# Kernel tuning notes

Hardware: AMD Instinct MI355X
Metric: run time of the kernel (lower is better)

The kernel has to match this reference:

```python
import jax, jax.numpy as jnp
import numpy as np

N, E, F_IN, D, B = 20000, 50000, 16, 64, 128


def setup_inputs() -> dict:
    key = jax.random.key(0)
    ks = jax.random.split(key, 24)
    s = 0.05
    inp = {
        "x": jax.random.normal(ks[0], (N, F_IN), jnp.float32),
        "edge_index": jax.random.randint(ks[1], (2, E), 0, N, jnp.int32),
        "edge_attr": jax.random.uniform(ks[2], (E, 5), jnp.float32),
        "batch": jnp.sort(jax.random.randint(ks[3], (N,), 0, B, jnp.int32)),
        # lin0
        "lin0_w": jax.random.normal(ks[4], (D, F_IN)) * s,
        "lin0_b": jnp.zeros((D,), jnp.float32),
        # edge MLP: Linear(5,128) -> ReLU -> Linear(128, D*D)
        "mlp_w1": jax.random.normal(ks[5], (128, 5)) * s,
        "mlp_b1": jnp.zeros((128,), jnp.float32),
        "mlp_w2": jax.random.normal(ks[6], (D * D, 128)) * s,
        "mlp_b2": jnp.zeros((D * D,), jnp.float32),
        # NNConv bias (root_weight=False, bias=True)
        "conv_b": jnp.zeros((D,), jnp.float32),
        # GRU(dim, dim), single layer
        "gru_w_ih": jax.random.normal(ks[7], (3 * D, D)) * s,
        "gru_w_hh": jax.random.normal(ks[8], (3 * D, D)) * s,
        "gru_b_ih": jnp.zeros((3 * D,), jnp.float32),
        "gru_b_hh": jnp.zeros((3 * D,), jnp.float32),
        # Set2Set LSTM(2*dim, dim)
        "lstm_w_ih": jax.random.normal(ks[9], (4 * D, 2 * D)) * s,
        "lstm_w_hh": jax.random.normal(ks[10], (4 * D, D)) * s,
        "lstm_b_ih": jnp.zeros((4 * D,), jnp.float32),
        "lstm_b_hh": jnp.zeros((4 * D,), jnp.float32),
    }
    return inp


def _gru_cell(x, h, w_ih, w_hh, b_ih, b_hh):
    gi = x @ w_ih.T + b_ih
    gh = h @ w_hh.T + b_hh
    i_r, i_z, i_n = jnp.split(gi, 3, axis=-1)
    h_r, h_z, h_n = jnp.split(gh, 3, axis=-1)
    r = jax.nn.sigmoid(i_r + h_r)
    z = jax.nn.sigmoid(i_z + h_z)
    n = jnp.tanh(i_n + r * h_n)
    return (1.0 - z) * n + z * h


def _lstm_cell(x, h, c, w_ih, w_hh, b_ih, b_hh):
    g = x @ w_ih.T + b_ih + h @ w_hh.T + b_hh
    i, f, gg, o = jnp.split(g, 4, axis=-1)
    c_new = jax.nn.sigmoid(f) * c + jax.nn.sigmoid(i) * jnp.tanh(gg)
    h_new = jax.nn.sigmoid(o) * jnp.tanh(c_new)
    return h_new, c_new


def reference(x, edge_index, edge_attr, batch,
              lin0_w, lin0_b, mlp_w1, mlp_b1, mlp_w2, mlp_b2, conv_b,
              gru_w_ih, gru_w_hh, gru_b_ih, gru_b_hh,
              lstm_w_ih, lstm_w_hh, lstm_b_ih, lstm_b_hh):
    src, dst = edge_index[0], edge_index[1]

    out = jax.nn.relu(x @ lin0_w.T + lin0_b)  # [N, D]
    h = out  # GRU hidden (seq_len=1 -> out == h after each step)

    # Edge-conditioned weights: MLP(edge_attr) -> [E, D, D]
    hidden = jax.nn.relu(edge_attr @ mlp_w1.T + mlp_b1)
    W_e = (hidden @ mlp_w2.T + mlp_b2).reshape(E, D, D)

    # in-degree counts for mean aggregation
    deg = jax.ops.segment_sum(jnp.ones((E,), x.dtype), dst, num_segments=N)
    deg = jnp.maximum(deg, 1.0)[:, None]

    for _ in range(3):
        # NNConv: gather src feats, per-edge matmul, scatter-mean to dst
        msg = jnp.einsum('ed,edo->eo', out[src], W_e)  # [E, D]
        agg = jax.ops.segment_sum(msg, dst, num_segments=N) / deg
        m = jax.nn.relu(agg + conv_b)
        h = _gru_cell(m, h, gru_w_ih, gru_w_hh, gru_b_ih, gru_b_hh)
        out = h

    # Set2Set pooling, 3 processing steps
    q_star = jnp.zeros((B, 2 * D), x.dtype)
    hh = jnp.zeros((B, D), x.dtype)
    cc = jnp.zeros((B, D), x.dtype)
    for _ in range(3):
        hh, cc = _lstm_cell(q_star, hh, cc, lstm_w_ih, lstm_w_hh, lstm_b_ih, lstm_b_hh)
        q = hh  # [B, D]
        e = jnp.sum(out * q[batch], axis=-1)  # [N]
        e_max = jax.ops.segment_max(e, batch, num_segments=B)
        a = jnp.exp(e - e_max[batch])
        a = a / jax.ops.segment_sum(a, batch, num_segments=B)[batch]
        r = jax.ops.segment_sum(a[:, None] * out, batch, num_segments=B)  # [B, D]
        q_star = jnp.concatenate([q, r], axis=-1)

    return q_star  # [B, 2*D]
```

## Files before the change

### kernel.cpp

```cpp
#include <hip/hip_runtime.h>
#include <hip/hip_bf16.h>

typedef float BF;
__device__ __forceinline__ float ldf(const BF* p, int i) { return p[i]; }

typedef _Float16 h8 __attribute__((ext_vector_type(8)));
typedef float f4 __attribute__((ext_vector_type(4)));

static constexpr int N_NODES = 20000;
static constexpr int N_EDGES = 50000;
static constexpr int E_PAD   = 50176;
static constexpr int N_MSGB  = 392;
static constexpr int N_PAD   = 20032;
static constexpr int BROW    = 136;
static constexpr int SROW    = 72;
static constexpr int N_B     = 79;
static constexpr int MAXSEG  = 2048;

__device__ __forceinline__ float sigf(float x) { return 1.f / (1.f + __expf(-x)); }
__device__ __forceinline__ float tanh_f(float x) {
  float e = __expf(2.f * x);
  return 1.f - 2.f / (e + 1.f);
}

static constexpr int S1_LIN0 = 5000;
static constexpr int S1_QS   = 2048;
static constexpr int S1_WCAT = 128;
static constexpr int S1_B2S  = 16;
static constexpr int S1_DEG  = 196;
static constexpr int PREP1_BLOCKS = S1_LIN0 + S1_QS + S1_WCAT + S1_B2S + 1 + 1 + S1_DEG;

__global__ void k_prep1(const BF* __restrict__ x, const int* __restrict__ batch,
                        const int* __restrict__ dst,
                        const BF* __restrict__ w0, const BF* __restrict__ b0,
                        const BF* __restrict__ w2, const BF* __restrict__ b2,
                        const BF* __restrict__ gwih, const BF* __restrict__ gwhh,
                        const BF* __restrict__ gbih, const BF* __restrict__ gbhh,
                        float* __restrict__ h, _Float16* __restrict__ h16,
                        _Float16* __restrict__ Qs, _Float16* __restrict__ Wcat,
                        float* __restrict__ bcat, _Float16* __restrict__ b2s,
                        int* __restrict__ seg, int* __restrict__ degi,
                        int* __restrict__ bsum) {
  int bid = blockIdx.x, t = threadIdx.x;
  if (bid < S1_LIN0) {
    __shared__ float xs[64];
    if (t < 64) xs[t] = ldf(x, bid * 64 + t);
    __syncthreads();
    int nl = t >> 6, o = t & 63;
    float acc = ldf(b0, o);
#pragma unroll
    for (int f = 0; f < 16; ++f) acc += xs[nl * 16 + f] * ldf(w0, o * 16 + f);
    float v = fmaxf(acc, 0.f);
    int idx = bid * 256 + t;
    h[idx] = v;
    h16[idx] = (_Float16)v;
    return;
  }
  bid -= S1_LIN0;
  if (bid < S1_QS) {
    int idx = bid * 256 + t;
#pragma unroll
    for (int rep = 0; rep < 1; ++rep) {
      int i = idx;
      int dl = i >> 13, rem = i & 8191;
      int f = rem >> 9, ln = (rem >> 3) & 63, j = i & 7;
      int o = (f & 3) * 16 + (ln & 15);
      int k = (f >> 2) * 32 + (ln >> 4) * 8 + j;
      Qs[i] = (_Float16)ldf(w2, (dl * 64 + o) * 128 + k);
    }
    return;
  }
  bid -= S1_QS;
  if (bid < S1_WCAT) {
    int idx = bid * 256 + t, row = idx >> 7, k = idx & 127;
    int g = row >> 6, rr = row & 63;
    float v = 0.f;
    if (g == 0) v = (k < 64) ? ldf(gwih, rr * 64 + k) : ldf(gwhh, rr * 64 + (k - 64));
    else if (g == 1) v = (k < 64) ? ldf(gwih, (64 + rr) * 64 + k) : ldf(gwhh, (64 + rr) * 64 + (k - 64));
    else if (g == 2) v = (k < 64) ? ldf(gwih, (128 + rr) * 64 + k) : 0.f;
    else v = (k < 64) ? 0.f : ldf(gwhh, (128 + rr) * 64 + (k - 64));
    Wcat[idx] = (_Float16)v;
    return;
  }
  bid -= S1_WCAT;
  if (bid < S1_B2S) {
    int idx = bid * 256 + t;
    int f = idx >> 9, ln = (idx >> 3) & 63, j = idx & 7;
    int o = (f & 3) * 16 + (ln & 15);
    int d = (f >> 2) * 32 + (ln >> 4) * 8 + j;
    b2s[idx] = (_Float16)ldf(b2, d * 64 + o);
    return;
  }
  bid -= S1_B2S;
  if (bid == 0) {
    float v;
    if (t < 128) v = ldf(gbih, t) + ldf(gbhh, t);
    else if (t < 192) v = ldf(gbih, t);
    else v = ldf(gbhh, t - 64);
    bcat[t] = v;
    return;
  }
  bid -= 1;
  if (bid == 0) {
    if (t > 128) return;
    if (t == 128) { seg[128] = N_NODES; return; }
    int lo = 0, hi = N_NODES;
    while (lo < hi) {
      int mid = (lo + hi) >> 1;
      if (batch[mid] < t) lo = mid + 1; else hi = mid;
    }
    seg[t] = lo;
    return;
  }
  bid -= 1;
  {
    int e = bid * 256 + t;
    if (e < N_EDGES) {
      int d = dst[e];
      atomicAdd(&degi[d], 1);
      atomicAdd(&bsum[d >> 8], 1);
    }
  }
}

__global__ void k_scanA(const int* __restrict__ bsum, int* __restrict__ boff) {
  __shared__ int sd[128];
  int t = threadIdx.x;
  int x = (t < N_B) ? bsum[t] : 0;
  sd[t] = x;
  __syncthreads();
#pragma unroll
  for (int o = 1; o < 128; o <<= 1) {
    int val = (t >= o) ? sd[t - o] : 0;
    __syncthreads();
    sd[t] += val;
    __syncthreads();
  }
  if (t < N_B) boff[t] = sd[t] - x;
}

__global__ void k_scanB(const int* __restrict__ degi, const int* __restrict__ boff,
                        int* __restrict__ cursor) {
  __shared__ int sd[256];
  int b = blockIdx.x, t = threadIdx.x;
  int v = b * 256 + t;
  int x = (v < N_NODES) ? degi[v] : 0;
  sd[t] = x;
  __syncthreads();
#pragma unroll
  for (int o = 1; o < 256; o <<= 1) {
    int val = (t >= o) ? sd[t - o] : 0;
    __syncthreads();
    sd[t] += val;
    __syncthreads();
  }
  if (v < N_NODES) cursor[v] = boff[b] + sd[t] - x;
}

__global__ void k_fill(const int* __restrict__ dst, int* __restrict__ cursor,
                       int* __restrict__ eperm) {
  int e = blockIdx.x * 256 + threadIdx.x;
  if (e < N_EDGES) {
    int pos = atomicAdd(&cursor[dst[e]], 1);
    eperm[pos] = e;
  }
}

static constexpr int S2_MLP = E_PAD / 2;
static constexpr int S2_SP  = 196;

__global__ void k_prep2(const BF* __restrict__ ea, const int* __restrict__ src,
                        const int* __restrict__ dst, const int* __restrict__ eperm,
                        const BF* __restrict__ w1, const BF* __restrict__ b1,
                        _Float16* __restrict__ hidf, int* __restrict__ spadp,
                        int* __restrict__ dpadp) {
  int bid = blockIdx.x, t = threadIdx.x;
  if (bid < S2_MLP) {
    __shared__ float eas[10];
    __shared__ int el2[2];
    if (t < 2) { int pos = bid * 2 + t; el2[t] = (pos < N_EDGES) ? eperm[pos] : -1; }
    __syncthreads();
    if (t < 10) { int e = el2[t / 5]; eas[t] = (e >= 0) ? ldf(ea, e * 5 + (t % 5)) : 0.f; }
    __syncthreads();
    int le = t >> 7, j = t & 127;
    int pos = bid * 2 + le;
    float v = 0.f;
    if (pos < N_EDGES) {
      float acc = ldf(b1, j);
#pragma unroll
      for (int i = 0; i < 5; ++i) acc += eas[le * 5 + i] * ldf(w1, j * 5 + i);
      v = fmaxf(acc, 0.f);
    }
    hidf[(size_t)pos * 128 + j] = (_Float16)v;
    return;
  }
  bid -= S2_MLP;
  {
    int pos = bid * 256 + t;
    if (pos < E_PAD) {
      int e = (pos < N_EDGES) ? eperm[pos] : -1;
      spadp[pos] = (e >= 0) ? src[e] : 0;
      dpadp[pos] = (e >= 0) ? dst[e] : 0;
    }
  }
}

__launch_bounds__(256, 2)
__global__ void k_msg(const _Float16* __restrict__ h16, const _Float16* __restrict__ hidf,
                      const _Float16* __restrict__ Qs, const _Float16* __restrict__ b2s,
                      const int* __restrict__ spadp, const int* __restrict__ dpadp,
                      float* __restrict__ agg) {
  __shared__ _Float16 s_lds[128 * SROW];
  __shared__ _Float16 b_lds[2][8192];
  __shared__ _Float16 b2l[4096];
  const int tid = threadIdx.x;
  const int wv = tid >> 6, ln = tid & 63;
  const int m0 = ln & 15, quad = ln >> 4;
  const int tb = blockIdx.x * 128;

  {
    int el = tid >> 1, half = (tid & 1) * 32;
    int sp_ = spadp[tb + el];
    const uint4* hp4 = (const uint4*)(h16 + (size_t)sp_ * 64 + half);
    uint4 a0 = hp4[0], a1 = hp4[1], a2 = hp4[2], a3 = hp4[3];
    *(uint4*)&s_lds[el * SROW + half] = a0;
    *(uint4*)&s_lds[el * SROW + half + 8] = a1;
    *(uint4*)&s_lds[el * SROW + half + 16] = a2;
    *(uint4*)&s_lds[el * SROW + half + 24] = a3;
  }
  {
    const uint4* sp4 = (const uint4*)b2s;
    *(uint4*)&b2l[tid * 16] = sp4[tid * 2];
    *(uint4*)&b2l[tid * 16 + 8] = sp4[tid * 2 + 1];
  }
  h8 hvv[2][4];
#pragma unroll
  for (int mt = 0; mt < 2; ++mt) {
    int e = tb + wv * 32 + mt * 16 + m0;
    const _Float16* hp = hidf + (size_t)e * 128 + quad * 8;
#pragma unroll
    for (int c = 0; c < 4; ++c) hvv[mt][c] = *(const h8*)(hp + c * 32);
  }
  uint4 breg[4];
  {
    const uint4* qb = (const uint4*)Qs;
#pragma unroll
    for (int c = 0; c < 4; ++c) breg[c] = qb[tid + c * 256];
#pragma unroll
    for (int c = 0; c < 4; ++c) *(uint4*)&b_lds[0][(tid + c * 256) * 8] = breg[c];
  }
  __syncthreads();

  f4 acc[2][4];
#pragma unroll
  for (int mt = 0; mt < 2; ++mt)
#pragma unroll
    for (int ct = 0; ct < 4; ++ct)
#pragma unroll
      for (int j = 0; j < 4; ++j) acc[mt][ct][j] = 0.f;

  for (int dl = 0; dl < 64; ++dl) {
    int cur = dl & 1;
    if (dl < 63) {
      const uint4* qb = (const uint4*)(Qs + (size_t)(dl + 1) * 8192);
#pragma unroll
      for (int c = 0; c < 4; ++c) breg[c] = qb[tid + c * 256];
    }
    _Float16 sv0 = s_lds[(wv * 32 + m0) * SROW + dl];
    _Float16 sv1 = s_lds[(wv * 32 + 16 + m0) * SROW + dl];
#pragma unroll
    for (int t = 0; t < 4; ++t) {
      h8 a0 = hvv[0][t] * sv0;
      h8 a1 = hvv[1][t] * sv1;
#pragma unroll
      for (int ct = 0; ct < 4; ++ct) {
        h8 b = *(const h8*)&b_lds[cur][(t * 4 + ct) * 512 + ln * 8];
        acc[0][ct] = __builtin_amdgcn_mfma_f32_16x16x32_f16(a0, b, acc[0][ct], 0, 0, 0);
        acc[1][ct] = __builtin_amdgcn_mfma_f32_16x16x32_f16(a1, b, acc[1][ct], 0, 0, 0);
      }
    }
    if (dl < 63) {
#pragma unroll
      for (int c = 0; c < 4; ++c) *(uint4*)&b_lds[cur ^ 1][(tid + c * 256) * 8] = breg[c];
    }
    __syncthreads();
  }
#pragma unroll
  for (int tp = 0; tp < 2; ++tp) {
    h8 a0 = *(const h8*)&s_lds[(wv * 32 + m0) * SROW + tp * 32 + quad * 8];
    h8 a1 = *(const h8*)&s_lds[(wv * 32 + 16 + m0) * SROW + tp * 32 + quad * 8];
#pragma unroll
    for (int ct = 0; ct < 4; ++ct) {
      h8 b = *(const h8*)&b2l[(tp * 4 + ct) * 512 + ln * 8];
      acc[0][ct] = __builtin_amdgcn_mfma_f32_16x16x32_f16(a0, b, acc[0][ct], 0, 0, 0);
      acc[1][ct] = __builtin_amdgcn_mfma_f32_16x16x32_f16(a1, b, acc[1][ct], 0, 0, 0);
    }
  }
#pragma unroll
  for (int mt = 0; mt < 2; ++mt) {
#pragma unroll
    for (int r = 0; r < 4; ++r) {
      int pos = tb + wv * 32 + mt * 16 + quad * 4 + r;
      if (pos < N_EDGES) {
        float* ap = agg + (size_t)dpadp[pos] * 64 + m0;
#pragma unroll
        for (int ct = 0; ct < 4; ++ct) atomicAdd(ap + ct * 16, acc[mt][ct][r]);
      }
    }
  }
}

__launch_bounds__(256)
__global__ void k_gru(float* __restrict__ agg, const int* __restrict__ degi,
                      const BF* __restrict__ convb, const _Float16* __restrict__ W,
                      const float* __restrict__ bcat, float* __restrict__ h,
                      _Float16* __restrict__ h16) {
  __shared__ _Float16 xa[64 * BROW];
  __shared__ _Float16 wb[256 * BROW];
  __shared__ float bsh[256];
  int tid = threadIdx.x;
  int wv = tid >> 6, ln = tid & 63, m0 = ln & 15, quad = ln >> 4;
  int rowblk = blockIdx.x * 64;
  bsh[tid] = bcat[tid];
  {
    int r = tid >> 2, c0 = (tid & 3) * 16;
    int node = rowblk + r;
    _Float16 mv[16], hv[16];
    if (node < N_NODES) {
      float inv = 1.f / (float)max(degi[node], 1);
      float* ap = agg + (size_t)node * 64 + c0;
      const float* hp = h + (size_t)node * 64 + c0;
#pragma unroll
      for (int i = 0; i < 16; i += 4) {
        float4 a = *(float4*)(ap + i);
        *(float4*)(ap + i) = make_float4(0.f, 0.f, 0.f, 0.f);
        float4 hf = *(const float4*)(hp + i);
        mv[i + 0] = (_Float16)fmaxf(a.x * inv + ldf(convb, c0 + i + 0), 0.f);
        mv[i + 1] = (_Float16)fmaxf(a.y * inv + ldf(convb, c0 + i + 1), 0.f);
        mv[i + 2] = (_Float16)fmaxf(a.z * inv + ldf(convb, c0 + i + 2), 0.f);
        mv[i + 3] = (_Float16)fmaxf(a.w * inv + ldf(convb, c0 + i + 3), 0.f);
        hv[i + 0] = (_Float16)hf.x; hv[i + 1] = (_Float16)hf.y;
        hv[i + 2] = (_Float16)hf.z; hv[i + 3] = (_Float16)hf.w;
      }
    } else {
#pragma unroll
      for (int i = 0; i < 16; ++i) { mv[i] = (_Float16)0.f; hv[i] = (_Float16)0.f; }
    }
    *(uint4*)&xa[r * BROW + c0] = *(const uint4*)&mv[0];
    *(uint4*)&xa[r * BROW + c0 + 8] = *(const uint4*)&mv[8];
    *(uint4*)&xa[r * BROW + 64 + c0] = *(const uint4*)&hv[0];
    *(uint4*)&xa[r * BROW + 64 + c0 + 8] = *(const uint4*)&hv[8];
  }
#pragma unroll
  for (int c = 0; c < 16; ++c) {
    int i = tid + c * 256, r = i >> 4, ch = i & 15;
    *(uint4*)&wb[r * BROW + ch * 8] = *(const uint4*)(W + (size_t)r * 128 + ch * 8);
  }
  __syncthreads();
  f4 acc[16];
#pragma unroll
  for (int ct = 0; ct < 16; ++ct)
#pragma unroll
    for (int j = 0; j < 4; ++j) acc[ct][j] = 0.f;
#pragma unroll
  for (int t = 0; t < 4; ++t) {
    h8 a = *(const h8*)&xa[(wv * 16 + m0) * BROW + t * 32 + quad * 8];
#pragma unroll
    for (int ct = 0; ct < 16; ++ct) {
      h8 b = *(const h8*)&wb[(ct * 16 + m0) * BROW + t * 32 + quad * 8];
      acc[ct] = __builtin_amdgcn_mfma_f32_16x16x32_f16(a, b, acc[ct], 0, 0, 0);
    }
  }
#pragma unroll
  for (int c0 = 0; c0 < 4; ++c0) {
    int o = c0 * 16 + m0;
    float br = bsh[o], bz = bsh[64 + o], bn = bsh[128 + o], bh2 = bsh[192 + o];
#pragma unroll
    for (int r = 0; r < 4; ++r) {
      int row = rowblk + wv * 16 + quad * 4 + r;
      if (row < N_NODES) {
        float rr = sigf(acc[c0][r] + br);
        float zz = sigf(acc[c0 + 4][r] + bz);
        float nn = tanh_f(acc[c0 + 8][r] + bn + rr * (acc[c0 + 12][r] + bh2));
        size_t hi = (size_t)row * 64 + o;
        float hp = h[hi];
        float hn = (1.f - zz) * nn + zz * hp;
        h[hi] = hn;
        h16[hi] = (_Float16)hn;
      }
    }
  }
}

__launch_bounds__(256)
__global__ void k_s2s(const float* __restrict__ h, const int* __restrict__ seg,
                      const BF* __restrict__ wih, const BF* __restrict__ whh,
                      const BF* __restrict__ bih, const BF* __restrict__ bhh,
                      float* __restrict__ outp) {
  __shared__ float xrow[128], g[256], qrow[64], hc[64], ccs[64], rr_[64];
  __shared__ float evals[MAXSEG];
  __shared__ float wred[4], rpart[256];
  int b = blockIdx.x, t = threadIdx.x;
  int wv = t >> 6, ln = t & 63;
  if (t < 64) { hc[t] = 0.f; ccs[t] = 0.f; rr_[t] = 0.f; }
  __syncthreads();
  int start = seg[b], end = seg[b + 1];
  int cnt = end - start;
  for (int st = 0; st < 3; ++st) {
    if (t < 64) xrow[t] = hc[t];
    else if (t < 128) xrow[t] = rr_[t - 64];
    __syncthreads();
    {
      float acc = ldf(bih, t) + ldf(bhh, t);
      const BF* wr = wih + t * 128;
      for (int i = 0; i < 128; ++i) acc += xrow[i] * ldf(wr, i);
      const BF* wr2 = whh + t * 64;
      for (int i = 0; i < 64; ++i) acc += xrow[i] * ldf(wr2, i);
      g[t] = acc;
    }
    __syncthreads();
    if (t < 64) {
      float ig = sigf(g[t]), fg = sigf(g[64 + t]);
      float gg = tanh_f(g[128 + t]), og = sigf(g[192 + t]);
      float c = fg * ccs[t] + ig * gg;
      ccs[t] = c;
      float hn = og * tanh_f(c);
      hc[t] = hn;
      qrow[t] = hn;
    }
    __syncthreads();
    float mw = -3.4e38f;
    for (int n = start + wv; n < end; n += 4) {
      float p = h[(size_t)n * 64 + ln] * qrow[ln];
#pragma unroll
      for (int off = 32; off > 0; off >>= 1) p += __shfl_xor(p, off);
      if (ln == 0) evals[n - start] = p;
      mw = fmaxf(mw, p);
    }
    if (ln == 0) wred[wv] = mw;
    __syncthreads();
    float gmax = fmaxf(fmaxf(wred[0], wred[1]), fmaxf(wred[2], wred[3]));
    __syncthreads();
    float psum = 0.f;
    for (int i = t; i < cnt; i += 256) {
      float a = __expf(evals[i] - gmax);
      evals[i] = a;
      psum += a;
    }
#pragma unroll
    for (int off = 32; off > 0; off >>= 1) psum += __shfl_xor(psum, off);
    if (ln == 0) wred[wv] = psum;
    __syncthreads();
    float inv = 1.f / fmaxf(wred[0] + wred[1] + wred[2] + wred[3], 1e-30f);
    float racc = 0.f;
    for (int n = start + wv; n < end; n += 4)
      racc += evals[n - start] * h[(size_t)n * 64 + ln];
    rpart[wv * 64 + ln] = racc;
    __syncthreads();
    if (t < 64)
      rr_[t] = (rpart[t] + rpart[64 + t] + rpart[128 + t] + rpart[192 + t]) * inv;
    __syncthreads();
  }
  if (t < 128) outp[b * 128 + t] = (t < 64) ? hc[t] : rr_[t - 64];
}

extern "C" void kernel_launch(void* const* d_in, const int* in_sizes, int n_in,
                              void* d_out, int out_size, void* d_ws, size_t ws_size,
                              hipStream_t stream) {
  const BF* x      = (const BF*)d_in[0];
  const int* ei    = (const int*)d_in[1];
  const BF* ea     = (const BF*)d_in[2];
  const int* batch = (const int*)d_in[3];
  const BF* w0     = (const BF*)d_in[4];
  const BF* b0     = (const BF*)d_in[5];
  const BF* w1     = (const BF*)d_in[6];
  const BF* b1     = (const BF*)d_in[7];
  const BF* w2     = (const BF*)d_in[8];
  const BF* b2     = (const BF*)d_in[9];
  const BF* convb  = (const BF*)d_in[10];
  const BF* gwih   = (const BF*)d_in[11];
  const BF* gwhh   = (const BF*)d_in[12];
  const BF* gbih   = (const BF*)d_in[13];
  const BF* gbhh   = (const BF*)d_in[14];
  const BF* lwih   = (const BF*)d_in[15];
  const BF* lwhh   = (const BF*)d_in[16];
  const BF* lbih   = (const BF*)d_in[17];
  const BF* lbhh   = (const BF*)d_in[18];
  const int* src = ei;
  const int* dstp = ei + N_EDGES;

  char* w = (char*)d_ws;
  size_t off_b = 0;
  auto take = [&](size_t bytes) -> void* {
    void* p = w + off_b;
    off_b = (off_b + bytes + 255) & ~(size_t)255;
    return p;
  };
  _Float16* Qs   = (_Float16*)take((size_t)4096 * 128 * 2);
  _Float16* hidf = (_Float16*)take((size_t)E_PAD * 128 * 2);
  float* h       = (float*)take((size_t)N_NODES * 64 * 4);
  _Float16* h16  = (_Float16*)take((size_t)N_NODES * 64 * 2);
  float* zr      = (float*)take((size_t)(N_NODES * 64 + N_NODES + 128) * 4);
  float* agg     = zr;
  int*   degi    = (int*)(zr + N_NODES * 64);
  int*   bsum    = degi + N_NODES;
  _Float16* Wcat = (_Float16*)take((size_t)256 * 128 * 2);
  float* bcat    = (float*)take((size_t)256 * 4);
  _Float16* b2s  = (_Float16*)take((size_t)8 * 512 * 2);
  int*   seg     = (int*)take((size_t)129 * 4);
  int*   boff    = (int*)take((size_t)128 * 4);
  int*   cursor  = (int*)take((size_t)N_NODES * 4);
  int*   eperm   = (int*)take((size_t)N_EDGES * 4);
  int*   spadp   = (int*)take((size_t)E_PAD * 4);
  int*   dpadp   = (int*)take((size_t)E_PAD * 4);

  hipMemsetAsync(zr, 0, (size_t)(N_NODES * 64 + N_NODES + 128) * 4, stream);
  k_prep1<<<PREP1_BLOCKS, 256, 0, stream>>>(x, batch, dstp, w0, b0, w2, b2,
                                            gwih, gwhh, gbih, gbhh,
                                            h, h16, Qs, Wcat, bcat, b2s,
                                            seg, degi, bsum);
  k_scanA<<<1, 128, 0, stream>>>(bsum, boff);
  k_scanB<<<N_B, 256, 0, stream>>>(degi, boff, cursor);
  k_fill<<<196, 256, 0, stream>>>(dstp, cursor, eperm);
  k_prep2<<<S2_MLP + S2_SP, 256, 0, stream>>>(ea, src, dstp, eperm, w1, b1,
                                              hidf, spadp, dpadp);
  for (int it = 0; it < 3; ++it) {
    k_msg<<<N_MSGB, 256, 0, stream>>>(h16, hidf, Qs, b2s, spadp, dpadp, agg);
    k_gru<<<N_PAD / 64, 256, 0, stream>>>(agg, degi, convb, Wcat, bcat, h, h16);
  }
  k_s2s<<<128, 256, 0, stream>>>(h, seg, lwih, lwhh, lbih, lbhh, (float*)d_out);
}
```

Baseline: 509.4 us.

## Widen Set2Set kernel to 1024 threads with two-node unrolled reductions

The Set2Set pooling kernel now runs with 1024 threads per graph (16 wavefronts) instead of 256. Each wavefront handles two nodes per iteration in the attention-score and readout loops. The LSTM gate matvec now reads weights as float4, and the per-wave reductions grow to 16 partials. The aim is more memory-level parallelism on a kernel that only launches 128 blocks, at the cost of larger blocks, more reduction work and a leftover cosmetic loop cleanup.

```diff
diff --git a/kernel.cpp b/kernel.cpp
--- a/kernel.cpp
+++ b/kernel.cpp
@@ -58,16 +58,12 @@
   }
   bid -= S1_LIN0;
   if (bid < S1_QS) {
-    int idx = bid * 256 + t;
-#pragma unroll
-    for (int rep = 0; rep < 1; ++rep) {
-      int i = idx;
-      int dl = i >> 13, rem = i & 8191;
-      int f = rem >> 9, ln = (rem >> 3) & 63, j = i & 7;
-      int o = (f & 3) * 16 + (ln & 15);
-      int k = (f >> 2) * 32 + (ln >> 4) * 8 + j;
-      Qs[i] = (_Float16)ldf(w2, (dl * 64 + o) * 128 + k);
-    }
+    int i = bid * 256 + t;
+    int dl = i >> 13, rem = i & 8191;
+    int f = rem >> 9, ln = (rem >> 3) & 63, j = i & 7;
+    int o = (f & 3) * 16 + (ln & 15);
+    int k = (f >> 2) * 32 + (ln >> 4) * 8 + j;
+    Qs[i] = (_Float16)ldf(w2, (dl * 64 + o) * 128 + k);
     return;
   }
   bid -= S1_QS;
@@ -392,14 +388,14 @@
   }
 }
 
-__launch_bounds__(256)
+__launch_bounds__(1024)
 __global__ void k_s2s(const float* __restrict__ h, const int* __restrict__ seg,
                       const BF* __restrict__ wih, const BF* __restrict__ whh,
                       const BF* __restrict__ bih, const BF* __restrict__ bhh,
                       float* __restrict__ outp) {
   __shared__ float xrow[128], g[256], qrow[64], hc[64], ccs[64], rr_[64];
   __shared__ float evals[MAXSEG];
-  __shared__ float wred[4], rpart[256];
+  __shared__ float wred[16], wred2[16], rpart[16 * 64];
   int b = blockIdx.x, t = threadIdx.x;
   int wv = t >> 6, ln = t & 63;
   if (t < 64) { hc[t] = 0.f; ccs[t] = 0.f; rr_[t] = 0.f; }
@@ -410,12 +406,22 @@
     if (t < 64) xrow[t] = hc[t];
     else if (t < 128) xrow[t] = rr_[t - 64];
     __syncthreads();
-    {
+    if (t < 256) {
       float acc = ldf(bih, t) + ldf(bhh, t);
-      const BF* wr = wih + t * 128;
-      for (int i = 0; i < 128; ++i) acc += xrow[i] * ldf(wr, i);
-      const BF* wr2 = whh + t * 64;
-      for (int i = 0; i < 64; ++i) acc += xrow[i] * ldf(wr2, i);
+      const float4* wr4 = (const float4*)(wih + t * 128);
+#pragma unroll
+      for (int i = 0; i < 32; ++i) {
+        float4 wv4 = wr4[i];
+        acc += xrow[i * 4] * wv4.x + xrow[i * 4 + 1] * wv4.y +
+               xrow[i * 4 + 2] * wv4.z + xrow[i * 4 + 3] * wv4.w;
+      }
+      const float4* wr2 = (const float4*)(whh + t * 64);
+#pragma unroll
+      for (int i = 0; i < 16; ++i) {
+        float4 wv4 = wr2[i];
+        acc += xrow[i * 4] * wv4.x + xrow[i * 4 + 1] * wv4.y +
+               xrow[i * 4 + 2] * wv4.z + xrow[i * 4 + 3] * wv4.w;
+      }
       g[t] = acc;
     }
     __syncthreads();
@@ -429,36 +435,58 @@
       qrow[t] = hn;
     }
     __syncthreads();
+    float q = qrow[ln];
     float mw = -3.4e38f;
-    for (int n = start + wv; n < end; n += 4) {
-      float p = h[(size_t)n * 64 + ln] * qrow[ln];
-#pragma unroll
-      for (int off = 32; off > 0; off >>= 1) p += __shfl_xor(p, off);
-      if (ln == 0) evals[n - start] = p;
-      mw = fmaxf(mw, p);
+    for (int n0 = start + wv * 2; n0 < end; n0 += 32) {
+      int n1 = n0 + 1;
+      float p0 = h[(size_t)n0 * 64 + ln] * q;
+      float p1 = (n1 < end) ? h[(size_t)n1 * 64 + ln] * q : 0.f;
+#pragma unroll
+      for (int off = 32; off > 0; off >>= 1) {
+        p0 += __shfl_xor(p0, off);
+        p1 += __shfl_xor(p1, off);
+      }
+      if (ln == 0) {
+        evals[n0 - start] = p0;
+        mw = fmaxf(mw, p0);
+        if (n1 < end) { evals[n1 - start] = p1; mw = fmaxf(mw, p1); }
+      }
     }
     if (ln == 0) wred[wv] = mw;
     __syncthreads();
-    float gmax = fmaxf(fmaxf(wred[0], wred[1]), fmaxf(wred[2], wred[3]));
+    float gmax = -3.4e38f;
+#pragma unroll
+    for (int i = 0; i < 16; ++i) gmax = fmaxf(gmax, wred[i]);
     __syncthreads();
     float psum = 0.f;
-    for (int i = t; i < cnt; i += 256) {
+    for (int i = t; i < cnt; i += 1024) {
       float a = __expf(evals[i] - gmax);
       evals[i] = a;
       psum += a;
     }
 #pragma unroll
     for (int off = 32; off > 0; off >>= 1) psum += __shfl_xor(psum, off);
-    if (ln == 0) wred[wv] = psum;
-    __syncthreads();
-    float inv = 1.f / fmaxf(wred[0] + wred[1] + wred[2] + wred[3], 1e-30f);
+    if (ln == 0) wred2[wv] = psum;
+    __syncthreads();
+    float tsum = 0.f;
+#pragma unroll
+    for (int i = 0; i < 16; ++i) tsum += wred2[i];
+    float inv = 1.f / fmaxf(tsum, 1e-30f);
     float racc = 0.f;
-    for (int n = start + wv; n < end; n += 4)
-      racc += evals[n - start] * h[(size_t)n * 64 + ln];
+    for (int n0 = start + wv * 2; n0 < end; n0 += 32) {
+      int n1 = n0 + 1;
+      float a0 = evals[n0 - start] * h[(size_t)n0 * 64 + ln];
+      float a1 = (n1 < end) ? evals[n1 - start] * h[(size_t)n1 * 64 + ln] : 0.f;
+      racc += a0 + a1;
+    }
     rpart[wv * 64 + ln] = racc;
     __syncthreads();
-    if (t < 64)
-      rr_[t] = (rpart[t] + rpart[64 + t] + rpart[128 + t] + rpart[192 + t]) * inv;
+    if (t < 64) {
+      float s = 0.f;
+#pragma unroll
+      for (int i = 0; i < 16; ++i) s += rpart[i * 64 + t];
+      rr_[t] = s * inv;
+    }
     __syncthreads();
   }
   if (t < 128) outp[b * 128 + t] = (t < 64) ? hc[t] : rr_[t - 64];
@@ -528,5 +556,5 @@
     k_msg<<<N_MSGB, 256, 0, stream>>>(h16, hidf, Qs, b2s, spadp, dpadp, agg);
     k_gru<<<N_PAD / 64, 256, 0, stream>>>(agg, degi, convb, Wcat, bcat, h, h16);
   }
-  k_s2s<<<128, 256, 0, stream>>>(h, seg, lwih, lwhh, lbih, lbhh, (float*)d_out);
-}
+  k_s2s<<<128, 1024, 0, stream>>>(h, seg, lwih, lwhh, lbih, lbhh, (float*)d_out);
+}
```

New measurement: 467.5 us. 1.09x faster.
